# Performance work log

Hardware: AMD Instinct MI355X
Metric: run time of the kernel (lower is better)

## Reference

```python
import jax, jax.numpy as jnp
import numpy as np

WINDOW = 512      # sliding window size (causal: keys in [m-WINDOW+1, m])
NEG_INF = -1e30   # large negative instead of -inf for fp16/bf16 safety


def setup_inputs() -> dict:
    key = jax.random.key(0)
    kq, kk, kv = jax.random.split(key, 3)
    B, S, H, Hk, D = 1, 8192, 32, 8, 128
    q = jax.random.normal(kq, (B, S, H, D), dtype=jnp.float32)
    k = jax.random.normal(kk, (B, S, Hk, D), dtype=jnp.float32)
    v = jax.random.normal(kv, (B, S, Hk, D), dtype=jnp.float32)
    return {"q": q, "k": k, "v": v}


def _swa_causal(q, k, v, window):
    """Causal sliding-window attention with GQA, banded (no SxS matrix)."""
    B, S, H, D = q.shape
    Hk = k.shape[2]
    G = H // Hk                      # query heads per kv head
    C = window                        # query block size
    nb = S // C                       # number of query blocks (S divisible by C here)
    L = 2 * window - 1                # kv window width per query block
    pad = window - 1
    scale = 1.0 / jnp.sqrt(jnp.asarray(D, q.dtype))

    # pad keys/values at the front so every block can gather a full window
    kp = jnp.pad(k, ((0, 0), (pad, 0), (0, 0), (0, 0)))
    vp = jnp.pad(v, ((0, 0), (pad, 0), (0, 0), (0, 0)))

    # block queries: [B, nb, C, Hk, G, D]
    qb = q.reshape(B, nb, C, Hk, G, D)

    # kv windows: block n sees padded positions [n*C, n*C + L)
    starts = jnp.arange(nb) * C                      # [nb]
    idx = starts[:, None] + jnp.arange(L)[None, :]   # [nb, L] padded coords
    kw = kp[:, idx]                                  # [B, nb, L, Hk, D]
    vw = vp[:, idx]                                  # [B, nb, L, Hk, D]

    # banded scores: [B, nb, Hk, G, C, L]
    scores = jnp.einsum('bnchgd,bnlhd->bnhgcl', qb, kw) * scale

    # mask: query i (global m = n*C + i), kv slot j (global n_pos = n*C + j - pad)
    # causal window: i <= j <= i + window - 1 ; plus n_pos >= 0
    i = jnp.arange(C)
    j = jnp.arange(L)
    band = (j[None, :] >= i[:, None]) & (j[None, :] <= i[:, None] + window - 1)  # [C, L]
    valid_n = (starts[:, None] + j[None, :] - pad) >= 0                          # [nb, L]
    mask = band[None, :, :] & valid_n[:, None, :]                                # [nb, C, L]

    scores = jnp.where(mask[:, None, None, :, :][None], scores, NEG_INF)
    p = jax.nn.softmax(scores, axis=-1)              # [B, nb, Hk, G, C, L]

    o = jnp.einsum('bnhgcl,bnlhd->bnchgd', p, vw)    # [B, nb, C, Hk, G, D]
    return o.reshape(B, S, H, D)


def reference(q, k, v):
    return _swa_causal(q, k, v, WINDOW)
```

## Files before the change

### kernel.cpp

```cpp
#include <hip/hip_runtime.h>

#define NH   32
#define NHK  8
#define D    128
#define QB   64
#define KB   64
#define NT   128

typedef float f32x16 __attribute__((ext_vector_type(16)));
typedef short bf16x8 __attribute__((ext_vector_type(8)));
typedef unsigned int uint4v __attribute__((ext_vector_type(4)));

__device__ __forceinline__ unsigned cvtpk(float lo, float hi) {
  unsigned r;
  asm("v_cvt_pk_bf16_f32 %0, %1, %2" : "=v"(r) : "v"(lo), "v"(hi));
  return r;
}
__device__ __forceinline__ void gload16(const void* g, void* l) {
  __builtin_amdgcn_global_load_lds(
      (__attribute__((address_space(1))) void*)g,
      (__attribute__((address_space(3))) void*)l, 16, 0, 0);
}

__device__ __forceinline__ int kidx(int j, int col) {
  return (((j >> 1) << 8) + ((j & 1) << 7) + col) ^ (((j >> 1) & 15) << 3);
}
__device__ __forceinline__ int vidx(int d, int j) {
  return (((d >> 1) << 7) + ((d & 1) << 6) + j) ^ (((d >> 1) & 15) << 3);
}

__global__ __launch_bounds__(256)
void prep_kv(const float* __restrict__ kg, const float* __restrict__ vg,
             short* __restrict__ kpre, short* __restrict__ vpre)
{
  int blk = blockIdx.x;
  int tid = threadIdx.x;
  bool isV = blk >= (NHK * NT);
  int lb   = isV ? blk - NHK * NT : blk;
  int hk   = lb >> 7;
  int t    = lb & 127;
  if (!isV) {
    int j  = tid >> 2;
    int dq = (tid & 3) * 32;
    const float* kp = kg + ((size_t)(t*KB + j) * NHK + hk) * D + dq;
    short* dst = kpre + (((size_t)(hk*NT + t)) << 13);
    #pragma unroll
    for (int c = 0; c < 4; ++c) {
      float4 a  = *(const float4*)(kp + c*8);
      float4 b2 = *(const float4*)(kp + c*8 + 4);
      uint4v u;
      u[0] = cvtpk(a.x, a.y);   u[1] = cvtpk(a.z, a.w);
      u[2] = cvtpk(b2.x, b2.y); u[3] = cvtpk(b2.z, b2.w);
      *(uint4v*)&dst[kidx(j, dq + c*8)] = u;
    }
  } else {
    int d0 = (tid & 31) * 4;
    int j0 = (tid >> 5) * 8;
    float tv[8][4];
    #pragma unroll
    for (int r = 0; r < 8; ++r) {
      float4 x = *(const float4*)(vg + ((size_t)(t*KB + j0 + r) * NHK + hk) * D + d0);
      tv[r][0]=x.x; tv[r][1]=x.y; tv[r][2]=x.z; tv[r][3]=x.w;
    }
    short* dst = vpre + (((size_t)(hk*NT + t)) << 13);
    #pragma unroll
    for (int c = 0; c < 4; ++c) {
      int d = d0 + c;
      uint4v u;
      u[0] = cvtpk(tv[0][c], tv[1][c]);
      u[1] = cvtpk(tv[2][c], tv[3][c]);
      u[2] = cvtpk(tv[4][c], tv[5][c]);
      u[3] = cvtpk(tv[6][c], tv[7][c]);
      *(uint4v*)&dst[vidx(d, j0)] = u;
    }
  }
}

__global__ __launch_bounds__(128, 2)
void swa_fwd(const float* __restrict__ qg, const short* __restrict__ kpre,
             const short* __restrict__ vpre, float* __restrict__ og)
{
  __shared__ __align__(16) short lds_k[KB * D];
  __shared__ __align__(16) short lds_v[KB * D];

  const int tid  = threadIdx.x;
  const int lane = tid & 63;
  const int w    = tid >> 6;
  const int il   = lane & 31;
  const int half = lane >> 5;

  int b    = blockIdx.x;
  int lidx = (b & 7) * 512 + (b >> 3);
  int hk   = lidx >> 9;
  int rem  = lidx & 511;
  int bq   = rem >> 2;
  int h    = hk * 4 + (rem & 3);
  int qs   = bq * QB;

  const float qscale = 0.088388347648318447f * 1.4426950408889634f;

  bf16x8 qf[8];
  {
    const float* qp = qg + ((size_t)(qs + 32*w + il) * NH + h) * D + half * 8;
    #pragma unroll
    for (int ks = 0; ks < 8; ++ks) {
      float4 a = *(const float4*)(qp + ks*16);
      float4 c = *(const float4*)(qp + ks*16 + 4);
      uint4v u;
      u[0] = cvtpk(a.x*qscale, a.y*qscale);
      u[1] = cvtpk(a.z*qscale, a.w*qscale);
      u[2] = cvtpk(c.x*qscale, c.y*qscale);
      u[3] = cvtpk(c.z*qscale, c.w*qscale);
      qf[ks] = __builtin_bit_cast(bf16x8, u);
    }
  }

  f32x16 acc_o[4];
  #pragma unroll
  for (int dt = 0; dt < 4; ++dt)
    #pragma unroll
    for (int r = 0; r < 16; ++r) acc_o[dt][r] = 0.0f;

  float l0 = 0.0f, l1 = 0.0f, l2 = 0.0f, l3 = 0.0f;

  int t_lo = bq - 8; if (t_lo < 0) t_lo = 0;
  int t_hi = bq;
  const int iw_min = qs + 32*w;

  const short* gkb = kpre + (((size_t)hk * NT) << 13);
  const short* gvb = vpre + (((size_t)hk * NT) << 13);
  const int lo = w * 4096;
  const int go = lo + lane * 8;

  for (int t = t_lo; t <= t_hi; ++t) {
    const int kt = t * KB;

    {
      const short* gk = gkb + ((size_t)t << 13);
      const short* gv = gvb + ((size_t)t << 13);
      #pragma unroll
      for (int i = 0; i < 8; ++i) gload16(gk + go + i*512, &lds_k[0] + lo + i*512);
      #pragma unroll
      for (int i = 0; i < 8; ++i) gload16(gv + go + i*512, &lds_v[0] + lo + i*512);
    }
    asm volatile("s_waitcnt vmcnt(0)" ::: "memory");
    __builtin_amdgcn_s_barrier();
    __builtin_amdgcn_sched_barrier(0);

    bool skip = (kt > iw_min + 31) || (kt + KB - 1 < iw_min - 511);
    if (!skip) {
      f32x16 acc_s[2];
      #pragma unroll
      for (int mt = 0; mt < 2; ++mt)
        #pragma unroll
        for (int r = 0; r < 16; ++r) acc_s[mt][r] = 0.0f;

      __builtin_amdgcn_s_setprio(1);
      #pragma unroll
      for (int ks = 0; ks < 8; ++ks) {
        #pragma unroll
        for (int mt = 0; mt < 2; ++mt) {
          int jrow = mt*32 + il;
          bf16x8 a = *(const bf16x8*)&lds_k[kidx(jrow, ks*16 + half*8)];
          acc_s[mt] = __builtin_amdgcn_mfma_f32_32x32x16_bf16(a, qf[ks], acc_s[mt], 0, 0, 0);
        }
      }
      __builtin_amdgcn_s_setprio(0);

      bool do_causal = (kt + KB - 1 > iw_min);
      bool do_window = (kt < iw_min + 31 - 511);
      if (do_causal || do_window) {
        int base0 = kt - iw_min - il + 4*half;
        #pragma unroll
        for (int mt = 0; mt < 2; ++mt)
          #pragma unroll
          for (int r = 0; r < 16; ++r) {
            int delta = base0 + 32*mt + (r & 3) + 8*(r >> 2);
            if ((do_causal && delta > 0) || (do_window && delta < -511))
              acc_s[mt][r] = -1e30f;
          }
      }

      #pragma unroll
      for (int mt = 0; mt < 2; ++mt) {
        float p[16];
        #pragma unroll
        for (int r = 0; r < 16; ++r)
          p[r] = __builtin_amdgcn_exp2f(acc_s[mt][r]);
        l0 += p[0] + p[4];  l1 += p[1] + p[5];
        l2 += p[2] + p[6];  l3 += p[3] + p[7];
        l0 += p[8] + p[12]; l1 += p[9] + p[13];
        l2 += p[10]+ p[14]; l3 += p[11]+ p[15];

        unsigned pkw[8];
        #pragma unroll
        for (int hb = 0; hb < 2; ++hb) {
          int bs = hb * 8;
          unsigned X1 = cvtpk(p[bs+0], p[bs+1]);
          unsigned X2 = cvtpk(p[bs+2], p[bs+3]);
          unsigned Y1 = cvtpk(p[bs+4], p[bs+5]);
          unsigned Y2 = cvtpk(p[bs+6], p[bs+7]);
          asm("v_permlane32_swap_b32 %0, %1" : "+v"(X1), "+v"(Y1));
          asm("v_permlane32_swap_b32 %0, %1" : "+v"(X2), "+v"(Y2));
          pkw[hb*4 + 0] = X1; pkw[hb*4 + 1] = X2;
          pkw[hb*4 + 2] = Y1; pkw[hb*4 + 3] = Y2;
        }
        __builtin_amdgcn_s_setprio(1);
        #pragma unroll
        for (int ksl = 0; ksl < 2; ++ksl) {
          int ks = mt*2 + ksl;
          uint4v pu;
          pu[0] = pkw[ksl*4+0]; pu[1] = pkw[ksl*4+1];
          pu[2] = pkw[ksl*4+2]; pu[3] = pkw[ksl*4+3];
          bf16x8 pb = __builtin_bit_cast(bf16x8, pu);
          #pragma unroll
          for (int dt = 0; dt < 4; ++dt) {
            int d = dt*32 + il;
            bf16x8 a = *(const bf16x8*)&lds_v[vidx(d, ks*16 + half*8)];
            acc_o[dt] = __builtin_amdgcn_mfma_f32_32x32x16_bf16(a, pb, acc_o[dt], 0, 0, 0);
          }
        }
        __builtin_amdgcn_s_setprio(0);
      }
    }
    if (t < t_hi) __builtin_amdgcn_s_barrier();
  }

  float l_lane = (l0 + l1) + (l2 + l3);
  float l_tot  = l_lane + __shfl_xor(l_lane, 32);
  float inv_l  = 1.0f / l_tot;
  const size_t orow = ((size_t)(qs + 32*w + il) * NH + h) * D;
  #pragma unroll
  for (int dt = 0; dt < 4; ++dt)
    #pragma unroll
    for (int rg = 0; rg < 4; ++rg) {
      float4 o;
      o.x = acc_o[dt][rg*4+0] * inv_l;
      o.y = acc_o[dt][rg*4+1] * inv_l;
      o.z = acc_o[dt][rg*4+2] * inv_l;
      o.w = acc_o[dt][rg*4+3] * inv_l;
      *(float4*)(og + orow + dt*32 + 8*rg + 4*half) = o;
    }
}

__global__ __launch_bounds__(256, 2)
void swa_fwd_fb(const float* __restrict__ qg, const float* __restrict__ kg,
                const float* __restrict__ vg, float* __restrict__ og)
{
  __shared__ __align__(16) short lds_k[KB * D];
  __shared__ __align__(16) short lds_v[D * KB];

  const int tid  = threadIdx.x;
  const int lane = tid & 63;
  const int w    = tid >> 6;
  const int il   = lane & 31;
  const int half = lane >> 5;

  int b    = blockIdx.x;
  int lidx = (b & 7) * 256 + (b >> 3);
  int hk   = lidx >> 8;
  int rem  = lidx & 255;
  int bq   = rem >> 2;
  int h    = hk * 4 + (rem & 3);
  int qs   = bq * 128;

  const float qscale = 0.088388347648318447f * 1.4426950408889634f;

  bf16x8 qf[8];
  {
    const float* qp = qg + ((size_t)(qs + 32*w + il) * NH + h) * D + half * 8;
    #pragma unroll
    for (int ks = 0; ks < 8; ++ks) {
      float4 a = *(const float4*)(qp + ks*16);
      float4 c = *(const float4*)(qp + ks*16 + 4);
      uint4v u;
      u[0] = cvtpk(a.x*qscale, a.y*qscale);
      u[1] = cvtpk(a.z*qscale, a.w*qscale);
      u[2] = cvtpk(c.x*qscale, c.y*qscale);
      u[3] = cvtpk(c.z*qscale, c.w*qscale);
      qf[ks] = __builtin_bit_cast(bf16x8, u);
    }
  }

  f32x16 acc_o[4];
  #pragma unroll
  for (int dt = 0; dt < 4; ++dt)
    #pragma unroll
    for (int r = 0; r < 16; ++r) acc_o[dt][r] = 0.0f;

  float l0 = 0.0f, l1 = 0.0f, l2 = 0.0f, l3 = 0.0f;

  int t_lo = 2*bq - 8; if (t_lo < 0) t_lo = 0;
  int t_hi = 2*bq + 1;
  const int iw_min = qs + 32*w;

  for (int t = t_lo; t <= t_hi; ++t) {
    const int kt = t * KB;
    {
      int j  = tid >> 2;
      int dq = (tid & 3) * 32;
      const float* kp = kg + ((size_t)(kt + j) * NHK + hk) * D + dq;
      #pragma unroll
      for (int c = 0; c < 4; ++c) {
        float4 a  = *(const float4*)(kp + c*8);
        float4 d2 = *(const float4*)(kp + c*8 + 4);
        uint4v u;
        u[0] = cvtpk(a.x, a.y);   u[1] = cvtpk(a.z, a.w);
        u[2] = cvtpk(d2.x, d2.y); u[3] = cvtpk(d2.z, d2.w);
        *(uint4v*)&lds_k[kidx(j, dq + c*8)] = u;
      }
    }
    {
      int d0 = (tid & 31) * 4;
      int j0 = (tid >> 5) * 8;
      float tv[8][4];
      #pragma unroll
      for (int r = 0; r < 8; ++r) {
        float4 x = *(const float4*)(vg + ((size_t)(kt + j0 + r) * NHK + hk) * D + d0);
        tv[r][0]=x.x; tv[r][1]=x.y; tv[r][2]=x.z; tv[r][3]=x.w;
      }
      #pragma unroll
      for (int c = 0; c < 4; ++c) {
        int d = d0 + c;
        uint4v u;
        u[0] = cvtpk(tv[0][c], tv[1][c]);
        u[1] = cvtpk(tv[2][c], tv[3][c]);
        u[2] = cvtpk(tv[4][c], tv[5][c]);
        u[3] = cvtpk(tv[6][c], tv[7][c]);
        *(uint4v*)&lds_v[vidx(d, j0)] = u;
      }
    }
    __syncthreads();

    bool skip = (kt > iw_min + 31) || (kt + KB - 1 < iw_min - 511);
    if (!skip) {
      f32x16 acc_s[2];
      #pragma unroll
      for (int mt = 0; mt < 2; ++mt)
        #pragma unroll
        for (int r = 0; r < 16; ++r) acc_s[mt][r] = 0.0f;

      #pragma unroll
      for (int ks = 0; ks < 8; ++ks) {
        #pragma unroll
        for (int mt = 0; mt < 2; ++mt) {
          int jrow = mt*32 + il;
          bf16x8 a = *(const bf16x8*)&lds_k[kidx(jrow, ks*16 + half*8)];
          acc_s[mt] = __builtin_amdgcn_mfma_f32_32x32x16_bf16(a, qf[ks], acc_s[mt], 0, 0, 0);
        }
      }

      bool do_causal = (kt + KB - 1 > iw_min);
      bool do_window = (kt < iw_min + 31 - 511);
      if (do_causal || do_window) {
        int base0 = kt - iw_min - il + 4*half;
        #pragma unroll
        for (int mt = 0; mt < 2; ++mt)
          #pragma unroll
          for (int r = 0; r < 16; ++r) {
            int delta = base0 + 32*mt + (r & 3) + 8*(r >> 2);
            if ((do_causal && delta > 0) || (do_window && delta < -511))
              acc_s[mt][r] = -1e30f;
          }
      }

      #pragma unroll
      for (int mt = 0; mt < 2; ++mt) {
        float p[16];
        #pragma unroll
        for (int r = 0; r < 16; ++r)
          p[r] = __builtin_amdgcn_exp2f(acc_s[mt][r]);
        l0 += p[0] + p[4];  l1 += p[1] + p[5];
        l2 += p[2] + p[6];  l3 += p[3] + p[7];
        l0 += p[8] + p[12]; l1 += p[9] + p[13];
        l2 += p[10]+ p[14]; l3 += p[11]+ p[15];

        unsigned pkw[8];
        #pragma unroll
        for (int hb = 0; hb < 2; ++hb) {
          int bs = hb * 8;
          unsigned X1 = cvtpk(p[bs+0], p[bs+1]);
          unsigned X2 = cvtpk(p[bs+2], p[bs+3]);
          unsigned Y1 = cvtpk(p[bs+4], p[bs+5]);
          unsigned Y2 = cvtpk(p[bs+6], p[bs+7]);
          asm("v_permlane32_swap_b32 %0, %1" : "+v"(X1), "+v"(Y1));
          asm("v_permlane32_swap_b32 %0, %1" : "+v"(X2), "+v"(Y2));
          pkw[hb*4 + 0] = X1; pkw[hb*4 + 1] = X2;
          pkw[hb*4 + 2] = Y1; pkw[hb*4 + 3] = Y2;
        }
        #pragma unroll
        for (int ksl = 0; ksl < 2; ++ksl) {
          int ks = mt*2 + ksl;
          uint4v pu;
          pu[0] = pkw[ksl*4+0]; pu[1] = pkw[ksl*4+1];
          pu[2] = pkw[ksl*4+2]; pu[3] = pkw[ksl*4+3];
          bf16x8 pb = __builtin_bit_cast(bf16x8, pu);
          #pragma unroll
          for (int dt = 0; dt < 4; ++dt) {
            int d = dt*32 + il;
            bf16x8 a = *(const bf16x8*)&lds_v[vidx(d, ks*16 + half*8)];
            acc_o[dt] = __builtin_amdgcn_mfma_f32_32x32x16_bf16(a, pb, acc_o[dt], 0, 0, 0);
          }
        }
      }
    }
    __syncthreads();
  }

  float l_lane = (l0 + l1) + (l2 + l3);
  float l_tot  = l_lane + __shfl_xor(l_lane, 32);
  float inv_l  = 1.0f / l_tot;
  const size_t orow = ((size_t)(qs + 32*w + il) * NH + h) * D;
  #pragma unroll
  for (int dt = 0; dt < 4; ++dt)
    #pragma unroll
    for (int rg = 0; rg < 4; ++rg) {
      float4 o;
      o.x = acc_o[dt][rg*4+0] * inv_l;
      o.y = acc_o[dt][rg*4+1] * inv_l;
      o.z = acc_o[dt][rg*4+2] * inv_l;
      o.w = acc_o[dt][rg*4+3] * inv_l;
      *(float4*)(og + orow + dt*32 + 8*rg + 4*half) = o;
    }
}

extern "C" void kernel_launch(void* const* d_in, const int* in_sizes, int n_in,
                              void* d_out, int out_size, void* d_ws, size_t ws_size,
                              hipStream_t stream) {
  const float* q = (const float*)d_in[0];
  const float* k = (const float*)d_in[1];
  const float* v = (const float*)d_in[2];
  float* o = (float*)d_out;
  const size_t per = (size_t)NHK * NT * KB * D;
  const size_t need = 2 * per * sizeof(short);
  if (ws_size >= need) {
    short* kpre = (short*)d_ws;
    short* vpre = kpre + per;
    hipLaunchKernelGGL(prep_kv, dim3(2 * NHK * NT), dim3(256), 0, stream, k, v, kpre, vpre);
    hipLaunchKernelGGL(swa_fwd, dim3(4096), dim3(128), 0, stream, q, kpre, vpre, o);
  } else {
    hipLaunchKernelGGL(swa_fwd_fb, dim3(2048), dim3(256), 0, stream, q, k, v, o);
  }
}
```

Before: 146.9 us.

## Switch main SWA kernel to 16x16x32 MFMA with four waves per block

Rewrites the main attention kernel to use 16x16x32 bf16 MFMA tiles, with 4 waves each owning 16 query rows instead of 2 waves owning 32 rows. K/V tile loads are now shared across 4 waves, and the skip granularity is finer, since each wave's window check covers 16 rows. Launch bounds move to 256 threads and 3 blocks per CU to raise occupancy through smaller accumulators. The trade-off is more MFMA instructions and lane-permute work per tile, plus an extra cross-lane reduction for the row sums.

```diff
diff --git a/kernel.cpp b/kernel.cpp
--- a/kernel.cpp
+++ b/kernel.cpp
@@ -7,7 +7,7 @@
 #define KB   64
 #define NT   128
 
-typedef float f32x16 __attribute__((ext_vector_type(16)));
+typedef float f32x4 __attribute__((ext_vector_type(4)));
 typedef short bf16x8 __attribute__((ext_vector_type(8)));
 typedef unsigned int uint4v __attribute__((ext_vector_type(4)));
 
@@ -76,7 +76,7 @@
   }
 }
 
-__global__ __launch_bounds__(128, 2)
+__global__ __launch_bounds__(256, 3)
 void swa_fwd(const float* __restrict__ qg, const short* __restrict__ kpre,
              const short* __restrict__ vpre, float* __restrict__ og)
 {
@@ -86,8 +86,8 @@
   const int tid  = threadIdx.x;
   const int lane = tid & 63;
   const int w    = tid >> 6;
-  const int il   = lane & 31;
-  const int half = lane >> 5;
+  const int il16 = lane & 15;
+  const int g    = lane >> 4;
 
   int b    = blockIdx.x;
   int lidx = (b & 7) * 512 + (b >> 3);
@@ -96,6 +96,165 @@
   int bq   = rem >> 2;
   int h    = hk * 4 + (rem & 3);
   int qs   = bq * QB;
+
+  const float qscale = 0.088388347648318447f * 1.4426950408889634f;
+
+  bf16x8 qf[4];
+  {
+    const float* qp = qg + ((size_t)(qs + 16*w + il16) * NH + h) * D + 8*g;
+    #pragma unroll
+    for (int ks = 0; ks < 4; ++ks) {
+      float4 a = *(const float4*)(qp + 32*ks);
+      float4 c = *(const float4*)(qp + 32*ks + 4);
+      uint4v u;
+      u[0] = cvtpk(a.x*qscale, a.y*qscale);
+      u[1] = cvtpk(a.z*qscale, a.w*qscale);
+      u[2] = cvtpk(c.x*qscale, c.y*qscale);
+      u[3] = cvtpk(c.z*qscale, c.w*qscale);
+      qf[ks] = __builtin_bit_cast(bf16x8, u);
+    }
+  }
+
+  f32x4 acc_o[8];
+  #pragma unroll
+  for (int dt = 0; dt < 8; ++dt)
+    #pragma unroll
+    for (int r = 0; r < 4; ++r) acc_o[dt][r] = 0.0f;
+
+  float l0 = 0.0f, l1 = 0.0f, l2 = 0.0f, l3 = 0.0f;
+
+  const int iw_min = qs + 16*w;
+  int t_lo = qs >= 512 ? (qs - 512) >> 6 : 0;
+  int t_hi = qs >> 6;
+
+  const short* gkb = kpre + (((size_t)hk * NT) << 13);
+  const short* gvb = vpre + (((size_t)hk * NT) << 13);
+  const int lo = w * 2048;
+  const int go = lo + lane * 8;
+
+  for (int t = t_lo; t <= t_hi; ++t) {
+    const int kt = t * KB;
+
+    {
+      const short* gk = gkb + ((size_t)t << 13);
+      const short* gv = gvb + ((size_t)t << 13);
+      #pragma unroll
+      for (int i = 0; i < 4; ++i) gload16(gk + go + i*512, &lds_k[0] + lo + i*512);
+      #pragma unroll
+      for (int i = 0; i < 4; ++i) gload16(gv + go + i*512, &lds_v[0] + lo + i*512);
+    }
+    asm volatile("s_waitcnt vmcnt(0)" ::: "memory");
+    __builtin_amdgcn_s_barrier();
+    __builtin_amdgcn_sched_barrier(0);
+
+    bool skip = (kt > iw_min + 15) || (kt + KB - 1 < iw_min - 511);
+    if (!skip) {
+      f32x4 acc_s[4];
+      #pragma unroll
+      for (int jt = 0; jt < 4; ++jt)
+        #pragma unroll
+        for (int r = 0; r < 4; ++r) acc_s[jt][r] = 0.0f;
+
+      __builtin_amdgcn_s_setprio(1);
+      #pragma unroll
+      for (int ks = 0; ks < 4; ++ks) {
+        #pragma unroll
+        for (int jt = 0; jt < 4; ++jt) {
+          bf16x8 a = *(const bf16x8*)&lds_k[kidx(16*jt + il16, 32*ks + 8*g)];
+          acc_s[jt] = __builtin_amdgcn_mfma_f32_16x16x32_bf16(a, qf[ks], acc_s[jt], 0, 0, 0);
+        }
+      }
+      __builtin_amdgcn_s_setprio(0);
+
+      bool do_causal = (kt + KB - 1 > iw_min);
+      bool do_window = (kt < iw_min + 15 - 511);
+      if (do_causal || do_window) {
+        int base0 = kt - iw_min + 4*g - il16;
+        #pragma unroll
+        for (int jt = 0; jt < 4; ++jt)
+          #pragma unroll
+          for (int r = 0; r < 4; ++r) {
+            int delta = base0 + 16*jt + r;
+            if ((do_causal && delta > 0) || (do_window && delta < -511))
+              acc_s[jt][r] = -1e30f;
+          }
+      }
+
+      float p[4][4];
+      #pragma unroll
+      for (int jt = 0; jt < 4; ++jt)
+        #pragma unroll
+        for (int r = 0; r < 4; ++r)
+          p[jt][r] = __builtin_amdgcn_exp2f(acc_s[jt][r]);
+      l0 += p[0][0] + p[1][0] + p[2][0] + p[3][0];
+      l1 += p[0][1] + p[1][1] + p[2][1] + p[3][1];
+      l2 += p[0][2] + p[1][2] + p[2][2] + p[3][2];
+      l3 += p[0][3] + p[1][3] + p[2][3] + p[3][3];
+
+      #pragma unroll
+      for (int kstep = 0; kstep < 2; ++kstep) {
+        unsigned A0 = cvtpk(p[2*kstep+0][0], p[2*kstep+0][1]);
+        unsigned B0 = cvtpk(p[2*kstep+0][2], p[2*kstep+0][3]);
+        unsigned C0 = cvtpk(p[2*kstep+1][0], p[2*kstep+1][1]);
+        unsigned D0 = cvtpk(p[2*kstep+1][2], p[2*kstep+1][3]);
+        asm("v_permlane32_swap_b32 %0, %1" : "+v"(A0), "+v"(C0));
+        asm("v_permlane32_swap_b32 %0, %1" : "+v"(B0), "+v"(D0));
+        asm("v_permlane16_swap_b32 %0, %1" : "+v"(A0), "+v"(C0));
+        asm("v_permlane16_swap_b32 %0, %1" : "+v"(B0), "+v"(D0));
+        uint4v pu; pu[0] = A0; pu[1] = B0; pu[2] = C0; pu[3] = D0;
+        bf16x8 pb = __builtin_bit_cast(bf16x8, pu);
+
+        __builtin_amdgcn_s_setprio(1);
+        #pragma unroll
+        for (int dt = 0; dt < 8; ++dt) {
+          bf16x8 a = *(const bf16x8*)&lds_v[vidx(16*dt + il16, 32*kstep + 8*g)];
+          acc_o[dt] = __builtin_amdgcn_mfma_f32_16x16x32_bf16(a, pb, acc_o[dt], 0, 0, 0);
+        }
+        __builtin_amdgcn_s_setprio(0);
+      }
+    }
+    if (t < t_hi) __builtin_amdgcn_s_barrier();
+  }
+
+  float l_lane = (l0 + l1) + (l2 + l3);
+  l_lane += __shfl_xor(l_lane, 16);
+  l_lane += __shfl_xor(l_lane, 32);
+  float inv_l = 1.0f / l_lane;
+
+  const size_t orow = ((size_t)(qs + 16*w + il16) * NH + h) * D;
+  #pragma unroll
+  for (int dt = 0; dt < 8; ++dt) {
+    float4 o;
+    o.x = acc_o[dt][0] * inv_l;
+    o.y = acc_o[dt][1] * inv_l;
+    o.z = acc_o[dt][2] * inv_l;
+    o.w = acc_o[dt][3] * inv_l;
+    *(float4*)(og + orow + 16*dt + 4*g) = o;
+  }
+}
+
+typedef float f32x16 __attribute__((ext_vector_type(16)));
+
+__global__ __launch_bounds__(256, 2)
+void swa_fwd_fb(const float* __restrict__ qg, const float* __restrict__ kg,
+                const float* __restrict__ vg, float* __restrict__ og)
+{
+  __shared__ __align__(16) short lds_k[KB * D];
+  __shared__ __align__(16) short lds_v[D * KB];
+
+  const int tid  = threadIdx.x;
+  const int lane = tid & 63;
+  const int w    = tid >> 6;
+  const int il   = lane & 31;
+  const int half = lane >> 5;
+
+  int b    = blockIdx.x;
+  int lidx = (b & 7) * 256 + (b >> 3);
+  int hk   = lidx >> 8;
+  int rem  = lidx & 255;
+  int bq   = rem >> 2;
+  int h    = hk * 4 + (rem & 3);
+  int qs   = bq * 128;
 
   const float qscale = 0.088388347648318447f * 1.4426950408889634f;
 
@@ -123,29 +282,47 @@
 
   float l0 = 0.0f, l1 = 0.0f, l2 = 0.0f, l3 = 0.0f;
 
-  int t_lo = bq - 8; if (t_lo < 0) t_lo = 0;
-  int t_hi = bq;
+  int t_lo = 2*bq - 8; if (t_lo < 0) t_lo = 0;
+  int t_hi = 2*bq + 1;
   const int iw_min = qs + 32*w;
-
-  const short* gkb = kpre + (((size_t)hk * NT) << 13);
-  const short* gvb = vpre + (((size_t)hk * NT) << 13);
-  const int lo = w * 4096;
-  const int go = lo + lane * 8;
 
   for (int t = t_lo; t <= t_hi; ++t) {
     const int kt = t * KB;
-
     {
-      const short* gk = gkb + ((size_t)t << 13);
-      const short* gv = gvb + ((size_t)t << 13);
-      #pragma unroll
-      for (int i = 0; i < 8; ++i) gload16(gk + go + i*512, &lds_k[0] + lo + i*512);
-      #pragma unroll
-      for (int i = 0; i < 8; ++i) gload16(gv + go + i*512, &lds_v[0] + lo + i*512);
-    }
-    asm volatile("s_waitcnt vmcnt(0)" ::: "memory");
-    __builtin_amdgcn_s_barrier();
-    __builtin_amdgcn_sched_barrier(0);
+      int j  = tid >> 2;
+      int dq = (tid & 3) * 32;
+      const float* kp = kg + ((size_t)(kt + j) * NHK + hk) * D + dq;
+      #pragma unroll
+      for (int c = 0; c < 4; ++c) {
+        float4 a  = *(const float4*)(kp + c*8);
+        float4 d2 = *(const float4*)(kp + c*8 + 4);
+        uint4v u;
+        u[0] = cvtpk(a.x, a.y);   u[1] = cvtpk(a.z, a.w);
+        u[2] = cvtpk(d2.x, d2.y); u[3] = cvtpk(d2.z, d2.w);
+        *(uint4v*)&lds_k[kidx(j, dq + c*8)] = u;
+      }
+    }
+    {
+      int d0 = (tid & 31) * 4;
+      int j0 = (tid >> 5) * 8;
+      float tv[8][4];
+      #pragma unroll
+      for (int r = 0; r < 8; ++r) {
+        float4 x = *(const float4*)(vg + ((size_t)(kt + j0 + r) * NHK + hk) * D + d0);
+        tv[r][0]=x.x; tv[r][1]=x.y; tv[r][2]=x.z; tv[r][3]=x.w;
+      }
+      #pragma unroll
+      for (int c = 0; c < 4; ++c) {
+        int d = d0 + c;
+        uint4v u;
+        u[0] = cvtpk(tv[0][c], tv[1][c]);
+        u[1] = cvtpk(tv[2][c], tv[3][c]);
+        u[2] = cvtpk(tv[4][c], tv[5][c]);
+        u[3] = cvtpk(tv[6][c], tv[7][c]);
+        *(uint4v*)&lds_v[vidx(d, j0)] = u;
+      }
+    }
+    __syncthreads();
 
     bool skip = (kt > iw_min + 31) || (kt + KB - 1 < iw_min - 511);
     if (!skip) {
@@ -155,7 +332,6 @@
         #pragma unroll
         for (int r = 0; r < 16; ++r) acc_s[mt][r] = 0.0f;
 
-      __builtin_amdgcn_s_setprio(1);
       #pragma unroll
       for (int ks = 0; ks < 8; ++ks) {
         #pragma unroll
@@ -165,7 +341,6 @@
           acc_s[mt] = __builtin_amdgcn_mfma_f32_32x32x16_bf16(a, qf[ks], acc_s[mt], 0, 0, 0);
         }
       }
-      __builtin_amdgcn_s_setprio(0);
 
       bool do_causal = (kt + KB - 1 > iw_min);
       bool do_window = (kt < iw_min + 31 - 511);
@@ -205,7 +380,6 @@
           pkw[hb*4 + 0] = X1; pkw[hb*4 + 1] = X2;
           pkw[hb*4 + 2] = Y1; pkw[hb*4 + 3] = Y2;
         }
-        __builtin_amdgcn_s_setprio(1);
         #pragma unroll
         for (int ksl = 0; ksl < 2; ++ksl) {
           int ks = mt*2 + ksl;
@@ -220,188 +394,6 @@
             acc_o[dt] = __builtin_amdgcn_mfma_f32_32x32x16_bf16(a, pb, acc_o[dt], 0, 0, 0);
           }
         }
-        __builtin_amdgcn_s_setprio(0);
-      }
-    }
-    if (t < t_hi) __builtin_amdgcn_s_barrier();
-  }
-
-  float l_lane = (l0 + l1) + (l2 + l3);
-  float l_tot  = l_lane + __shfl_xor(l_lane, 32);
-  float inv_l  = 1.0f / l_tot;
-  const size_t orow = ((size_t)(qs + 32*w + il) * NH + h) * D;
-  #pragma unroll
-  for (int dt = 0; dt < 4; ++dt)
-    #pragma unroll
-    for (int rg = 0; rg < 4; ++rg) {
-      float4 o;
-      o.x = acc_o[dt][rg*4+0] * inv_l;
-      o.y = acc_o[dt][rg*4+1] * inv_l;
-      o.z = acc_o[dt][rg*4+2] * inv_l;
-      o.w = acc_o[dt][rg*4+3] * inv_l;
-      *(float4*)(og + orow + dt*32 + 8*rg + 4*half) = o;
-    }
-}
-
-__global__ __launch_bounds__(256, 2)
-void swa_fwd_fb(const float* __restrict__ qg, const float* __restrict__ kg,
-                const float* __restrict__ vg, float* __restrict__ og)
-{
-  __shared__ __align__(16) short lds_k[KB * D];
-  __shared__ __align__(16) short lds_v[D * KB];
-
-  const int tid  = threadIdx.x;
-  const int lane = tid & 63;
-  const int w    = tid >> 6;
-  const int il   = lane & 31;
-  const int half = lane >> 5;
-
-  int b    = blockIdx.x;
-  int lidx = (b & 7) * 256 + (b >> 3);
-  int hk   = lidx >> 8;
-  int rem  = lidx & 255;
-  int bq   = rem >> 2;
-  int h    = hk * 4 + (rem & 3);
-  int qs   = bq * 128;
-
-  const float qscale = 0.088388347648318447f * 1.4426950408889634f;
-
-  bf16x8 qf[8];
-  {
-    const float* qp = qg + ((size_t)(qs + 32*w + il) * NH + h) * D + half * 8;
-    #pragma unroll
-    for (int ks = 0; ks < 8; ++ks) {
-      float4 a = *(const float4*)(qp + ks*16);
-      float4 c = *(const float4*)(qp + ks*16 + 4);
-      uint4v u;
-      u[0] = cvtpk(a.x*qscale, a.y*qscale);
-      u[1] = cvtpk(a.z*qscale, a.w*qscale);
-      u[2] = cvtpk(c.x*qscale, c.y*qscale);
-      u[3] = cvtpk(c.z*qscale, c.w*qscale);
-      qf[ks] = __builtin_bit_cast(bf16x8, u);
-    }
-  }
-
-  f32x16 acc_o[4];
-  #pragma unroll
-  for (int dt = 0; dt < 4; ++dt)
-    #pragma unroll
-    for (int r = 0; r < 16; ++r) acc_o[dt][r] = 0.0f;
-
-  float l0 = 0.0f, l1 = 0.0f, l2 = 0.0f, l3 = 0.0f;
-
-  int t_lo = 2*bq - 8; if (t_lo < 0) t_lo = 0;
-  int t_hi = 2*bq + 1;
-  const int iw_min = qs + 32*w;
-
-  for (int t = t_lo; t <= t_hi; ++t) {
-    const int kt = t * KB;
-    {
-      int j  = tid >> 2;
-      int dq = (tid & 3) * 32;
-      const float* kp = kg + ((size_t)(kt + j) * NHK + hk) * D + dq;
-      #pragma unroll
-      for (int c = 0; c < 4; ++c) {
-        float4 a  = *(const float4*)(kp + c*8);
-        float4 d2 = *(const float4*)(kp + c*8 + 4);
-        uint4v u;
-        u[0] = cvtpk(a.x, a.y);   u[1] = cvtpk(a.z, a.w);
-        u[2] = cvtpk(d2.x, d2.y); u[3] = cvtpk(d2.z, d2.w);
-        *(uint4v*)&lds_k[kidx(j, dq + c*8)] = u;
-      }
-    }
-    {
-      int d0 = (tid & 31) * 4;
-      int j0 = (tid >> 5) * 8;
-      float tv[8][4];
-      #pragma unroll
-      for (int r = 0; r < 8; ++r) {
-        float4 x = *(const float4*)(vg + ((size_t)(kt + j0 + r) * NHK + hk) * D + d0);
-        tv[r][0]=x.x; tv[r][1]=x.y; tv[r][2]=x.z; tv[r][3]=x.w;
-      }
-      #pragma unroll
-      for (int c = 0; c < 4; ++c) {
-        int d = d0 + c;
-        uint4v u;
-        u[0] = cvtpk(tv[0][c], tv[1][c]);
-        u[1] = cvtpk(tv[2][c], tv[3][c]);
-        u[2] = cvtpk(tv[4][c], tv[5][c]);
-        u[3] = cvtpk(tv[6][c], tv[7][c]);
-        *(uint4v*)&lds_v[vidx(d, j0)] = u;
-      }
-    }
-    __syncthreads();
-
-    bool skip = (kt > iw_min + 31) || (kt + KB - 1 < iw_min - 511);
-    if (!skip) {
-      f32x16 acc_s[2];
-      #pragma unroll
-      for (int mt = 0; mt < 2; ++mt)
-        #pragma unroll
-        for (int r = 0; r < 16; ++r) acc_s[mt][r] = 0.0f;
-
-      #pragma unroll
-      for (int ks = 0; ks < 8; ++ks) {
-        #pragma unroll
-        for (int mt = 0; mt < 2; ++mt) {
-          int jrow = mt*32 + il;
-          bf16x8 a = *(const bf16x8*)&lds_k[kidx(jrow, ks*16 + half*8)];
-          acc_s[mt] = __builtin_amdgcn_mfma_f32_32x32x16_bf16(a, qf[ks], acc_s[mt], 0, 0, 0);
-        }
-      }
-
-      bool do_causal = (kt + KB - 1 > iw_min);
-      bool do_window = (kt < iw_min + 31 - 511);
-      if (do_causal || do_window) {
-        int base0 = kt - iw_min - il + 4*half;
-        #pragma unroll
-        for (int mt = 0; mt < 2; ++mt)
-          #pragma unroll
-          for (int r = 0; r < 16; ++r) {
-            int delta = base0 + 32*mt + (r & 3) + 8*(r >> 2);
-            if ((do_causal && delta > 0) || (do_window && delta < -511))
-              acc_s[mt][r] = -1e30f;
-          }
-      }
-
-      #pragma unroll
-      for (int mt = 0; mt < 2; ++mt) {
-        float p[16];
-        #pragma unroll
-        for (int r = 0; r < 16; ++r)
-          p[r] = __builtin_amdgcn_exp2f(acc_s[mt][r]);
-        l0 += p[0] + p[4];  l1 += p[1] + p[5];
-        l2 += p[2] + p[6];  l3 += p[3] + p[7];
-        l0 += p[8] + p[12]; l1 += p[9] + p[13];
-        l2 += p[10]+ p[14]; l3 += p[11]+ p[15];
-
-        unsigned pkw[8];
-        #pragma unroll
-        for (int hb = 0; hb < 2; ++hb) {
-          int bs = hb * 8;
-          unsigned X1 = cvtpk(p[bs+0], p[bs+1]);
-          unsigned X2 = cvtpk(p[bs+2], p[bs+3]);
-          unsigned Y1 = cvtpk(p[bs+4], p[bs+5]);
-          unsigned Y2 = cvtpk(p[bs+6], p[bs+7]);
-          asm("v_permlane32_swap_b32 %0, %1" : "+v"(X1), "+v"(Y1));
-          asm("v_permlane32_swap_b32 %0, %1" : "+v"(X2), "+v"(Y2));
-          pkw[hb*4 + 0] = X1; pkw[hb*4 + 1] = X2;
-          pkw[hb*4 + 2] = Y1; pkw[hb*4 + 3] = Y2;
-        }
-        #pragma unroll
-        for (int ksl = 0; ksl < 2; ++ksl) {
-          int ks = mt*2 + ksl;
-          uint4v pu;
-          pu[0] = pkw[ksl*4+0]; pu[1] = pkw[ksl*4+1];
-          pu[2] = pkw[ksl*4+2]; pu[3] = pkw[ksl*4+3];
-          bf16x8 pb = __builtin_bit_cast(bf16x8, pu);
-          #pragma unroll
-          for (int dt = 0; dt < 4; ++dt) {
-            int d = dt*32 + il;
-            bf16x8 a = *(const bf16x8*)&lds_v[vidx(d, ks*16 + half*8)];
-            acc_o[dt] = __builtin_amdgcn_mfma_f32_32x32x16_bf16(a, pb, acc_o[dt], 0, 0, 0);
-          }
-        }
       }
     }
     __syncthreads();
@@ -437,7 +429,7 @@
     short* kpre = (short*)d_ws;
     short* vpre = kpre + per;
     hipLaunchKernelGGL(prep_kv, dim3(2 * NHK * NT), dim3(256), 0, stream, k, v, kpre, vpre);
-    hipLaunchKernelGGL(swa_fwd, dim3(4096), dim3(128), 0, stream, q, kpre, vpre, o);
+    hipLaunchKernelGGL(swa_fwd, dim3(4096), dim3(256), 0, stream, q, kpre, vpre, o);
   } else {
     hipLaunchKernelGGL(swa_fwd_fb, dim3(2048), dim3(256), 0, stream, q, k, v, o);
   }
```

Result: faster. 143.5 us (-2.3%).
